# Optimization experiments

Measured on AMD Instinct MI355X. Metric: run time of the kernel, lower is better.

The kernel has to match this reference:

```python
import jax, jax.numpy as jnp
import numpy as np

DIM, INNER, NH = 256, 64, 8
HD = INNER // NH  # 8
B, H, W = 2, 48, 48
EPS = 1e-6


def _ln2d(x, w, b):
    # channel-first LayerNorm over dim=1, biased variance (matches LayerNorm2d)
    u = x.mean(axis=1, keepdims=True)
    s = ((x - u) ** 2).mean(axis=1, keepdims=True)
    xn = (x - u) / jnp.sqrt(s + EPS)
    return w[None, :, None, None] * xn + b[None, :, None, None]


def _conv1x1(x, w, b):
    return jnp.einsum('oc,bchw->bohw', w, x) + b[None, :, None, None]


def _attn(q, k, v):
    # q,k,v: [B, INNER, H, W] -> global attention over HW tokens per head
    Bq, C, Hh, Ww = q.shape
    split = lambda t: t.reshape(Bq, NH, HD, Hh * Ww)
    q, k, v = split(q), split(k), split(v)
    scale = HD ** -0.5
    attn = jnp.einsum('bhdn,bhdm->bhnm', q, k) * scale  # [B,nh,HW,HW]
    attn = jax.nn.softmax(attn, axis=-1)
    out = jnp.einsum('bhnm,bhdm->bhdn', attn, v)
    return out.reshape(Bq, C, Hh, Ww)


def setup_inputs() -> dict:
    key = jax.random.key(0)
    ks = jax.random.split(key, 12)
    w = lambda k, o, i: jax.random.normal(k, (o, i), dtype=jnp.float32) * 0.02
    d = {
        'f_rgb': jax.random.normal(ks[0], (B, DIM, H, W), dtype=jnp.float32),
        'f_ir': jax.random.normal(ks[1], (B, DIM, H, W), dtype=jnp.float32),
        'nr_w': jnp.ones(DIM), 'nr_b': jnp.zeros(DIM),
        'ni_w': jnp.ones(DIM), 'ni_b': jnp.zeros(DIM),
        'qr_w': w(ks[2], INNER, DIM), 'qr_b': jnp.zeros(INNER),
        'kvi_w': w(ks[3], 2 * INNER, DIM), 'kvi_b': jnp.zeros(2 * INNER),
        'qi_w': w(ks[4], INNER, DIM), 'qi_b': jnp.zeros(INNER),
        'kvr_w': w(ks[5], 2 * INNER, DIM), 'kvr_b': jnp.zeros(2 * INNER),
        'pr_w': w(ks[6], DIM, INNER), 'pr_b': jnp.zeros(DIM),
        'pr_lnw': jnp.ones(DIM), 'pr_lnb': jnp.zeros(DIM),
        'pi_w': w(ks[7], DIM, INNER), 'pi_b': jnp.zeros(DIM),
        'pi_lnw': jnp.ones(DIM), 'pi_lnb': jnp.zeros(DIM),
        'gr_w': w(ks[8], DIM, 2 * DIM), 'gr_b': jnp.zeros(DIM),
        'gi_w': w(ks[9], DIM, 2 * DIM), 'gi_b': jnp.zeros(DIM),
    }
    return d


def reference(f_rgb, f_ir, nr_w, nr_b, ni_w, ni_b, qr_w, qr_b, kvi_w, kvi_b,
              qi_w, qi_b, kvr_w, kvr_b, pr_w, pr_b, pr_lnw, pr_lnb,
              pi_w, pi_b, pi_lnw, pi_lnb, gr_w, gr_b, gi_w, gi_b):
    n_rgb = _ln2d(f_rgb, nr_w, nr_b)
    n_ir = _ln2d(f_ir, ni_w, ni_b)

    # RGB queries attend to IR keys/values
    q_r = _conv1x1(n_rgb, qr_w, qr_b)
    kv_i = _conv1x1(n_ir, kvi_w, kvi_b)
    k_i, v_i = kv_i[:, :INNER], kv_i[:, INNER:]
    rgb_cross = _attn(q_r, k_i, v_i)
    rgb_cross = _ln2d(_conv1x1(rgb_cross, pr_w, pr_b), pr_lnw, pr_lnb)
    gate_r = jax.nn.sigmoid(_conv1x1(jnp.concatenate([f_rgb, rgb_cross], axis=1), gr_w, gr_b))
    f_rgb_out = f_rgb + gate_r * rgb_cross

    # IR queries attend to RGB keys/values
    q_i = _conv1x1(n_ir, qi_w, qi_b)
    kv_r = _conv1x1(n_rgb, kvr_w, kvr_b)
    k_r, v_r = kv_r[:, :INNER], kv_r[:, INNER:]
    ir_cross = _attn(q_i, k_r, v_r)
    ir_cross = _ln2d(_conv1x1(ir_cross, pi_w, pi_b), pi_lnw, pi_lnb)
    gate_i = jax.nn.sigmoid(_conv1x1(jnp.concatenate([f_ir, ir_cross], axis=1), gi_w, gi_b))
    f_ir_out = f_ir + gate_i * ir_cross

    return (f_rgb_out, f_ir_out)
```

## Files before the change

### kernel.cpp

```cpp
#include <hip/hip_runtime.h>

static constexpr int kDim   = 256;
static constexpr int kInner = 64;
static constexpr int kNH    = 8;
static constexpr int kB     = 2;
static constexpr int kP     = 2304;
static constexpr float kScaleL2 = 0.5100697891920077f;
static constexpr float kEps   = 1e-6f;

typedef __fp16   fp16x2 __attribute__((ext_vector_type(2)));
typedef _Float16 half4f __attribute__((ext_vector_type(4)));
typedef _Float16 half8  __attribute__((ext_vector_type(8)));
typedef float    f32x4  __attribute__((ext_vector_type(4)));

static constexpr size_t oXq  = 0;
static constexpr size_t oQ16 = 2359296;
static constexpr size_t oK16 = 2949120;
static constexpr size_t oV16 = 3538944;
static constexpr size_t oA16 = 4128768;
static constexpr size_t oW16 = 7077888;
static constexpr size_t kInpStride = 294912;

__global__ __launch_bounds__(256) void prep(
    const float* __restrict__ x0, const float* __restrict__ w0,
    const float* __restrict__ b0, const float* __restrict__ x1,
    const float* __restrict__ w1, const float* __restrict__ b1,
    _Float16* __restrict__ Xq,
    const float* __restrict__ qr_w, const float* __restrict__ kvr_w,
    const float* __restrict__ qi_w, const float* __restrict__ kvi_w,
    const float* __restrict__ pr_w, const float* __restrict__ pi_w,
    const float* __restrict__ gr_w, const float* __restrict__ gi_w,
    _Float16* __restrict__ w16)
{
    if (blockIdx.x >= 576) {
        const int flat = blockIdx.x - 576;
        const int y = flat >> 6, x = flat & 63;
        const float* src; _Float16* dst; int n;
        _Float16* Aq = w16;
        _Float16* Ap = w16 + 98304;
        _Float16* Ag = w16 + 131072;
        switch (y) {
            case 0: src = qr_w;  dst = Aq;          n = 16384;  break;
            case 1: src = kvr_w; dst = Aq + 16384;  n = 32768;  break;
            case 2: src = qi_w;  dst = Aq + 49152;  n = 16384;  break;
            case 3: src = kvi_w; dst = Aq + 65536;  n = 32768;  break;
            case 4: src = pr_w;  dst = Ap;          n = 16384;  break;
            case 5: src = pi_w;  dst = Ap + 16384;  n = 16384;  break;
            case 6: src = gr_w;  dst = Ag;          n = 131072; break;
            default:src = gi_w;  dst = Ag + 131072; n = 131072; break;
        }
        for (int i = x * 256 + threadIdx.x; i < n; i += 64 * 256)
            dst[i] = (_Float16)src[i];
        return;
    }
    __shared__ float sb[16][16];
    __shared__ float ssb[16][16];
    const int fid = blockIdx.x;
    const int xcd = fid & 7, q = fid >> 3;
    const int inp = (xcd >> 2) & 1, bb = (xcd >> 1) & 1, half = xcd & 1;
    const float* x = inp ? x1 : x0;
    const float* w = inp ? w1 : w0;
    const float* b = inp ? b1 : b0;
    const int pos = threadIdx.x & 15;
    const int grp = threadIdx.x >> 4;
    const int p   = half * 1152 + q * 16 + pos;
    const size_t base = (size_t)bb * kDim * kP + p;
    const int c0 = grp * 16;

    float v[16];
    float s = 0.f, ss = 0.f;
    #pragma unroll
    for (int j = 0; j < 16; ++j) {
        v[j] = x[base + (size_t)(c0 + j) * kP];
        s += v[j]; ss += v[j] * v[j];
    }
    sb[grp][pos] = s; ssb[grp][pos] = ss;
    __syncthreads();
    float st = 0.f, sst = 0.f;
    #pragma unroll
    for (int g = 0; g < 16; ++g) { st += sb[g][pos]; sst += ssb[g][pos]; }
    const float mean = st * (1.f / kDim);
    const float rstd = rsqrtf(sst * (1.f / kDim) - mean * mean + kEps);
    half8 h0, h1;
    #pragma unroll
    for (int j = 0; j < 8; ++j) {
        h0[j] = (_Float16)((v[j]     - mean) * rstd * w[c0 + j]     + b[c0 + j]);
        h1[j] = (_Float16)((v[j + 8] - mean) * rstd * w[c0 + j + 8] + b[c0 + j + 8]);
    }
    _Float16* dst = Xq + ((size_t)(inp * 2 + bb) * kP + p) * 256 + c0;
    *(half8*)dst       = h0;
    *(half8*)(dst + 8) = h1;
}

template <int M, int K, int EPI>
__global__ __launch_bounds__(256) void gemm_f16(
    const _Float16* __restrict__ A,
    const _Float16* __restrict__ B,
    const float* __restrict__ b0, const float* __restrict__ b1,
    const float* __restrict__ b2, const float* __restrict__ b3,
    _Float16* __restrict__ o16a, _Float16* __restrict__ o16b, _Float16* __restrict__ o16c,
    const float* __restrict__ f0, const float* __restrict__ f1,
    float* __restrict__ outp)
{
    constexpr int MT64 = M / 64;
    const int fid = blockIdx.x;
    const int xcd = fid & 7, q = fid >> 3;
    const int s = (xcd >> 2) & 1, bb = (xcd >> 1) & 1, half = xcd & 1;
    const int ot64 = (q % MT64) * 64;
    const int pt   = q / MT64;
    const int wv = threadIdx.x >> 6, lane = threadIdx.x & 63;
    const int r16 = lane & 15, g = lane >> 4;
    const int ot = ot64 + wv * 16;
    const int p0 = half * 1152 + pt * 64;
    const int combo = s * 2 + bb;

    const _Float16* Ar = A + ((size_t)s * M + ot + r16) * K + 8 * g;
    const _Float16* Br = B + ((size_t)combo * kP + p0 + r16) * K + 8 * g;
    f32x4 acc0[4], acc1[4];
    #pragma unroll
    for (int ps = 0; ps < 4; ++ps) {
        acc0[ps] = (f32x4){0.f, 0.f, 0.f, 0.f};
        acc1[ps] = (f32x4){0.f, 0.f, 0.f, 0.f};
    }
    #pragma unroll 4
    for (int c0 = 0; c0 < K; c0 += 32) {
        const half8 a8 = *(const half8*)(Ar + c0);
        half8 b8[4];
        #pragma unroll
        for (int ps = 0; ps < 4; ++ps)
            b8[ps] = *(const half8*)(Br + (size_t)(16 * ps) * K + c0);
        const half4f al = {a8[0], a8[1], a8[2], a8[3]};
        const half4f ah = {a8[4], a8[5], a8[6], a8[7]};
        #pragma unroll
        for (int ps = 0; ps < 4; ++ps) {
            const half4f bl = {b8[ps][0], b8[ps][1], b8[ps][2], b8[ps][3]};
            const half4f bh = {b8[ps][4], b8[ps][5], b8[ps][6], b8[ps][7]};
            acc0[ps] = __builtin_amdgcn_mfma_f32_16x16x16f16(al, bl, acc0[ps], 0, 0, 0);
            acc1[ps] = __builtin_amdgcn_mfma_f32_16x16x16f16(ah, bh, acc1[ps], 0, 0, 0);
        }
    }
    const int obase = ot + 4 * g;

    #pragma unroll
    for (int ps = 0; ps < 4; ++ps) {
        float acc[4];
        #pragma unroll
        for (int i = 0; i < 4; ++i) acc[i] = acc0[ps][i] + acc1[ps][i];
        const int p = p0 + 16 * ps + r16;

        if constexpr (EPI == 0) {
            const int dlo = 4 * (g & 1);
            if (ot < 64) {
                const float* qb = s ? b1 : b0;
                const float4 bv = *(const float4*)(qb + obase);
                const int h = (ot >> 3) + (g >> 1);
                half4f o = { (_Float16)((acc[0] + bv.x) * kScaleL2), (_Float16)((acc[1] + bv.y) * kScaleL2),
                             (_Float16)((acc[2] + bv.z) * kScaleL2), (_Float16)((acc[3] + bv.w) * kScaleL2) };
                *(half4f*)(o16a + (((size_t)combo * 8 + h) * kP + p) * 8 + dlo) = o;
            } else if (ot < 128) {
                const float* kb = s ? b3 : b2;
                const float4 bv = *(const float4*)(kb + obase - 64);
                const int h = ((ot - 64) >> 3) + (g >> 1);
                half4f o = { (_Float16)(acc[0] + bv.x), (_Float16)(acc[1] + bv.y),
                             (_Float16)(acc[2] + bv.z), (_Float16)(acc[3] + bv.w) };
                *(half4f*)(o16b + (((size_t)combo * 8 + h) * kP + p) * 8 + dlo) = o;
            } else {
                const float* kb = s ? b3 : b2;
                const float4 bv = *(const float4*)(kb + obase - 64);
                const int h = ((ot - 128) >> 3) + (g >> 1);
                const float* bvp = (const float*)&bv;
                #pragma unroll
                for (int i = 0; i < 4; ++i)
                    o16c[(((size_t)combo * 8 + h) * 8 + dlo + i) * kP + p] = (_Float16)(acc[i] + bvp[i]);
            }
        } else {
            const float* gb = s ? b1 : b0;
            const float4 bv = *(const float4*)(gb + obase);
            const float* bvp = (const float*)&bv;
            const half4f cx = *(const half4f*)(B + ((size_t)combo * kP + p) * 512 + 256 + obase);
            const float* F = s ? f1 : f0;
            #pragma unroll
            for (int i = 0; i < 4; ++i) {
                const int o = obase + i;
                const float gt = 1.f / (1.f + __expf(-(acc[i] + bvp[i])));
                const float fb = F[((size_t)bb * kDim + o) * kP + p];
                outp[((size_t)combo * kDim + o) * kP + p] = fb + gt * (float)cx[i];
            }
        }
    }
}

__global__ __launch_bounds__(256) void proj_ln(
    const _Float16* __restrict__ a16, const _Float16* __restrict__ Ap,
    const float* __restrict__ pb0, const float* __restrict__ pb1,
    const float* __restrict__ w0, const float* __restrict__ b0,
    const float* __restrict__ w1, const float* __restrict__ b1,
    const float* __restrict__ f0, const float* __restrict__ f1,
    _Float16* __restrict__ Xg)
{
    __shared__ float sb[4][4][16];
    __shared__ float ssb[4][4][16];
    const int fid = blockIdx.x;
    const int xcd = fid & 7, q = fid >> 3;
    const int s = (xcd >> 2) & 1, bb = (xcd >> 1) & 1, half = xcd & 1;
    const int wv = threadIdx.x >> 6, lane = threadIdx.x & 63;
    const int r16 = lane & 15, g = lane >> 4;
    const int p = half * 1152 + q * 16 + r16;
    const int combo = s * 2 + bb;
    const float* pb = s ? pb1 : pb0;
    const float* w  = s ? w1 : w0;
    const float* b  = s ? b1 : b0;
    const float* F  = s ? f1 : f0;

    const _Float16* Br = a16 + ((size_t)combo * kP + p) * 64 + 8 * g;
    const half8 bA = *(const half8*)Br;
    const half8 bB = *(const half8*)(Br + 32);
    const half4f bl0 = {bA[0], bA[1], bA[2], bA[3]};
    const half4f bh0 = {bA[4], bA[5], bA[6], bA[7]};
    const half4f bl1 = {bB[0], bB[1], bB[2], bB[3]};
    const half4f bh1 = {bB[4], bB[5], bB[6], bB[7]};

    float cval[4][4];
    float psum = 0.f, psq = 0.f;
    #pragma unroll
    for (int t = 0; t < 4; ++t) {
        const int ot = wv * 64 + t * 16;
        const _Float16* Ar = Ap + ((size_t)s * 256 + ot + r16) * 64 + 8 * g;
        const half8 aA = *(const half8*)Ar;
        const half8 aB = *(const half8*)(Ar + 32);
        const half4f al0 = {aA[0], aA[1], aA[2], aA[3]};
        const half4f ah0 = {aA[4], aA[5], aA[6], aA[7]};
        const half4f al1 = {aB[0], aB[1], aB[2], aB[3]};
        const half4f ah1 = {aB[4], aB[5], aB[6], aB[7]};
        f32x4 acc0 = __builtin_amdgcn_mfma_f32_16x16x16f16(al0, bl0, (f32x4){0.f,0.f,0.f,0.f}, 0, 0, 0);
        acc0 = __builtin_amdgcn_mfma_f32_16x16x16f16(al1, bl1, acc0, 0, 0, 0);
        f32x4 acc1 = __builtin_amdgcn_mfma_f32_16x16x16f16(ah0, bh0, (f32x4){0.f,0.f,0.f,0.f}, 0, 0, 0);
        acc1 = __builtin_amdgcn_mfma_f32_16x16x16f16(ah1, bh1, acc1, 0, 0, 0);
        const float4 bv = *(const float4*)(pb + ot + 4 * g);
        const float* bvp = (const float*)&bv;
        #pragma unroll
        for (int i = 0; i < 4; ++i) {
            const float v = acc0[i] + acc1[i] + bvp[i];
            cval[t][i] = v;
            psum += v; psq += v * v;
        }
    }
    sb[wv][g][r16] = psum; ssb[wv][g][r16] = psq;
    __syncthreads();
    float st = 0.f, sst = 0.f;
    #pragma unroll
    for (int w2 = 0; w2 < 4; ++w2)
        #pragma unroll
        for (int g2 = 0; g2 < 4; ++g2) { st += sb[w2][g2][r16]; sst += ssb[w2][g2][r16]; }
    const float mean = st * (1.f / kDim);
    const float rstd = rsqrtf(sst * (1.f / kDim) - mean * mean + kEps);

    _Float16* xrow = Xg + ((size_t)combo * kP + p) * 512;
    #pragma unroll
    for (int t = 0; t < 4; ++t) {
        const int o4 = wv * 64 + t * 16 + 4 * g;
        const float4 lw = *(const float4*)(w + o4);
        const float4 lb = *(const float4*)(b + o4);
        const float* lwp = (const float*)&lw;
        const float* lbp = (const float*)&lb;
        half4f o;
        #pragma unroll
        for (int i = 0; i < 4; ++i)
            o[i] = (_Float16)((cval[t][i] - mean) * rstd * lwp[i] + lbp[i]);
        *(half4f*)(xrow + 256 + o4) = o;
        half4f r;
        #pragma unroll
        for (int i = 0; i < 4; ++i)
            r[i] = (_Float16)F[((size_t)bb * kDim + o4 + i) * kP + p];
        *(half4f*)(xrow + o4) = r;
    }
}

__global__ __launch_bounds__(256) void attn_mfma(
    const _Float16* __restrict__ q16, const _Float16* __restrict__ k16,
    const _Float16* __restrict__ vt16, _Float16* __restrict__ a16)
{
    __shared__ _Float16 Ksm[16 * 64 * 4];
    __shared__ _Float16 Vsm[16 * 66 * 4];
    const int st = blockIdx.z;
    const _Float16* Qg = q16  + (size_t)st * kInpStride;
    const _Float16* Kg = k16  + (size_t)(1 - st) * kInpStride;
    const _Float16* Vg = vt16 + (size_t)(1 - st) * kInpStride;
    const int bh = blockIdx.y;
    const int bb = bh >> 3, h = bh & 7;
    const int tid  = threadIdx.x;
    const int wv   = tid >> 6;
    const int lane = tid & 63;
    const int r16  = lane & 15;
    const int g    = lane >> 4;

    #pragma unroll
    for (int j = 0; j < 2; ++j) {
        const int s = tid + 256 * j;
        const int kt = s >> 5, m = s & 31;
        *(half4f*)(Ksm + (kt * 64 + 32 + m) * 4) = (half4f){0, 0, 0, 0};
        const int rv = 8 + (m & 7), gv = m >> 3;
        const half4f vv = (rv == 8)
            ? (half4f){(_Float16)1.f, (_Float16)1.f, (_Float16)1.f, (_Float16)1.f}
            : (half4f){0, 0, 0, 0};
        *(half4f*)(Vsm + (kt * 66 + gv * 16 + rv) * 4) = vv;
    }

    const int qg = blockIdx.x * 64 + wv * 16 + r16;
    half4f qf = (half4f){0, 0, 0, 0};
    if (g < 2) qf = *(const half4f*)(Qg + ((size_t)bh * kP + qg) * 8 + g * 4);

    const int vd = tid >> 5, vc8 = (tid & 31) * 8;
    const int vkt = vc8 >> 4, vgv = (vc8 & 15) >> 2;
    _Float16* kdst = Ksm + ((tid >> 4) * 64 + (tid & 15)) * 4;
    _Float16* vdst = Vsm + (vkt * 66 + vgv * 16 + vd) * 4;
    const _Float16* ksrc = Kg + ((size_t)bh * kP + tid) * 8;
    const _Float16* vsrc = Vg + (size_t)(bh * 8 + vd) * kP + vc8;

    half8 kreg = *(const half8*)ksrc;
    half8 vreg = *(const half8*)vsrc;

    f32x4 of0 = (f32x4){0.f, 0.f, 0.f, 0.f};
    f32x4 of1 = (f32x4){0.f, 0.f, 0.f, 0.f};

    for (int ch = 0; ch < 9; ++ch) {
        if (ch) __syncthreads();
        *(half4f*)kdst        = (half4f){kreg[0], kreg[1], kreg[2], kreg[3]};
        *(half4f*)(kdst + 64) = (half4f){kreg[4], kreg[5], kreg[6], kreg[7]};
        *(half4f*)vdst        = (half4f){vreg[0], vreg[1], vreg[2], vreg[3]};
        *(half4f*)(vdst + 64) = (half4f){vreg[4], vreg[5], vreg[6], vreg[7]};
        __syncthreads();
        if (ch < 8) {
            kreg = *(const half8*)(ksrc + (size_t)(ch + 1) * 2048);
            vreg = *(const half8*)(vsrc + (size_t)(ch + 1) * 256);
        }
        #pragma unroll
        for (int kt = 0; kt < 16; ++kt) {
            const half4f kf = *(const half4f*)(Ksm + (kt * 64 + lane) * 4);
            f32x4 sv = __builtin_amdgcn_mfma_f32_16x16x16f16(kf, qf, (f32x4){0.f,0.f,0.f,0.f}, 0, 0, 0);
            const float e0 = exp2f(sv[0]), e1 = exp2f(sv[1]);
            const float e2 = exp2f(sv[2]), e3 = exp2f(sv[3]);
            const fp16x2 lo = __builtin_amdgcn_cvt_pkrtz(e0, e1);
            const fp16x2 hi = __builtin_amdgcn_cvt_pkrtz(e2, e3);
            const half4f pf = { (_Float16)lo[0], (_Float16)lo[1],
                                (_Float16)hi[0], (_Float16)hi[1] };
            const half4f vf = *(const half4f*)(Vsm + (kt * 66 + lane) * 4);
            if (kt & 1) of1 = __builtin_amdgcn_mfma_f32_16x16x16f16(vf, pf, of1, 0, 0, 0);
            else        of0 = __builtin_amdgcn_mfma_f32_16x16x16f16(vf, pf, of0, 0, 0, 0);
        }
    }
    const f32x4 of = of0 + of1;
    const float rsv = __shfl(of[0], 32 + r16, 64);
    const float inv = 1.f / rsv;
    if (g < 2) {
        half4f o = { (_Float16)(of[0] * inv), (_Float16)(of[1] * inv),
                     (_Float16)(of[2] * inv), (_Float16)(of[3] * inv) };
        *(half4f*)(a16 + ((size_t)(st * 2 + bb) * kP + qg) * 64 + h * 8 + g * 4) = o;
    }
}

extern "C" void kernel_launch(void* const* d_in, const int* in_sizes, int n_in,
                              void* d_out, int out_size, void* d_ws, size_t ws_size,
                              hipStream_t stream)
{
    const float* f_rgb  = (const float*)d_in[0];
    const float* f_ir   = (const float*)d_in[1];
    const float* nr_w   = (const float*)d_in[2];
    const float* nr_b   = (const float*)d_in[3];
    const float* ni_w   = (const float*)d_in[4];
    const float* ni_b   = (const float*)d_in[5];
    const float* qr_w   = (const float*)d_in[6];
    const float* qr_b   = (const float*)d_in[7];
    const float* kvi_w  = (const float*)d_in[8];
    const float* kvi_b  = (const float*)d_in[9];
    const float* qi_w   = (const float*)d_in[10];
    const float* qi_b   = (const float*)d_in[11];
    const float* kvr_w  = (const float*)d_in[12];
    const float* kvr_b  = (const float*)d_in[13];
    const float* pr_w   = (const float*)d_in[14];
    const float* pr_b   = (const float*)d_in[15];
    const float* pr_lnw = (const float*)d_in[16];
    const float* pr_lnb = (const float*)d_in[17];
    const float* pi_w   = (const float*)d_in[18];
    const float* pi_b   = (const float*)d_in[19];
    const float* pi_lnw = (const float*)d_in[20];
    const float* pi_lnb = (const float*)d_in[21];
    const float* gr_w   = (const float*)d_in[22];
    const float* gr_b   = (const float*)d_in[23];
    const float* gi_w   = (const float*)d_in[24];
    const float* gi_b   = (const float*)d_in[25];

    _Float16* hb   = (_Float16*)d_ws;
    _Float16* Xq   = hb + oXq;
    _Float16* q16  = hb + oQ16;
    _Float16* k16  = hb + oK16;
    _Float16* vt16 = hb + oV16;
    _Float16* a16  = hb + oA16;
    _Float16* Xg   = hb;
    _Float16* W16  = hb + oW16;
    _Float16* Aq   = W16;
    _Float16* Ap   = W16 + 98304;
    _Float16* Ag   = W16 + 131072;

    float* outp = (float*)d_out;
    const dim3 blk(256);

    prep<<<dim3(1088), blk, 0, stream>>>(f_rgb, nr_w, nr_b, f_ir, ni_w, ni_b, Xq,
                                         qr_w, kvr_w, qi_w, kvi_w, pr_w, pi_w, gr_w, gi_w, W16);
    gemm_f16<192, 256, 0><<<dim3(432), blk, 0, stream>>>(
        Aq, Xq, qr_b, qi_b, kvr_b, kvi_b, q16, k16, vt16, nullptr, nullptr, nullptr);
    attn_mfma<<<dim3(36, 16, 2), blk, 0, stream>>>(q16, k16, vt16, a16);
    proj_ln<<<dim3(576), blk, 0, stream>>>(a16, Ap, pr_b, pi_b,
                                           pr_lnw, pr_lnb, pi_lnw, pi_lnb,
                                           f_rgb, f_ir, Xg);
    gemm_f16<256, 512, 2><<<dim3(576), blk, 0, stream>>>(
        Ag, Xg, gr_b, gi_b, nullptr, nullptr, nullptr, nullptr, nullptr, f_rgb, f_ir, outp);
}
```

Baseline: 118.6 us.

## Double-buffer attention K/V tiles and process two query tiles per wave

```diff
diff --git a/kernel.cpp b/kernel.cpp
--- a/kernel.cpp
+++ b/kernel.cpp
@@ -280,8 +280,8 @@
     const _Float16* __restrict__ q16, const _Float16* __restrict__ k16,
     const _Float16* __restrict__ vt16, _Float16* __restrict__ a16)
 {
-    __shared__ _Float16 Ksm[16 * 64 * 4];
-    __shared__ _Float16 Vsm[16 * 66 * 4];
+    __shared__ _Float16 Ksm[2][8 * 512];
+    __shared__ _Float16 Vsm[2][8 * 528];
     const int st = blockIdx.z;
     const _Float16* Qg = q16  + (size_t)st * kInpStride;
     const _Float16* Kg = k16  + (size_t)(1 - st) * kInpStride;
@@ -295,67 +295,129 @@
     const int g    = lane >> 4;
 
     #pragma unroll
-    for (int j = 0; j < 2; ++j) {
-        const int s = tid + 256 * j;
-        const int kt = s >> 5, m = s & 31;
-        *(half4f*)(Ksm + (kt * 64 + 32 + m) * 4) = (half4f){0, 0, 0, 0};
-        const int rv = 8 + (m & 7), gv = m >> 3;
-        const half4f vv = (rv == 8)
-            ? (half4f){(_Float16)1.f, (_Float16)1.f, (_Float16)1.f, (_Float16)1.f}
-            : (half4f){0, 0, 0, 0};
-        *(half4f*)(Vsm + (kt * 66 + gv * 16 + rv) * 4) = vv;
-    }
-
-    const int qg = blockIdx.x * 64 + wv * 16 + r16;
-    half4f qf = (half4f){0, 0, 0, 0};
-    if (g < 2) qf = *(const half4f*)(Qg + ((size_t)bh * kP + qg) * 8 + g * 4);
-
+    for (int jb = 0; jb < 2; ++jb) {
+        #pragma unroll
+        for (int j = 0; j < 2; ++j) {
+            const int s = tid + 256 * j;
+            const int kt = s >> 5, m = s & 31;
+            *(half4f*)(Ksm[jb] + (kt >> 1) * 512 + (32 + m) * 8 + (kt & 1) * 4) = (half4f){0, 0, 0, 0};
+            const int rv = 8 + (m & 7), gv = m >> 3;
+            const half4f vvp = (rv == 8)
+                ? (half4f){(_Float16)1.f, (_Float16)1.f, (_Float16)1.f, (_Float16)1.f}
+                : (half4f){0, 0, 0, 0};
+            *(half4f*)(Vsm[jb] + (kt >> 1) * 528 + (gv * 16 + rv) * 8 + (kt & 1) * 4) = vvp;
+        }
+    }
+
+    const int qgA = blockIdx.x * 128 + wv * 16 + r16;
+    const int qgB = qgA + 64;
+    half4f qfA = (half4f){0, 0, 0, 0};
+    half4f qfB = (half4f){0, 0, 0, 0};
+    if (g < 2) {
+        qfA = *(const half4f*)(Qg + ((size_t)bh * kP + qgA) * 8 + g * 4);
+        qfB = *(const half4f*)(Qg + ((size_t)bh * kP + qgB) * 8 + g * 4);
+    }
+
+    const int kkt = tid >> 4, kr = tid & 15;
     const int vd = tid >> 5, vc8 = (tid & 31) * 8;
     const int vkt = vc8 >> 4, vgv = (vc8 & 15) >> 2;
-    _Float16* kdst = Ksm + ((tid >> 4) * 64 + (tid & 15)) * 4;
-    _Float16* vdst = Vsm + (vkt * 66 + vgv * 16 + vd) * 4;
+    const int koff  = (kkt >> 1) * 512 + kr * 8 + (kkt & 1) * 4;
+    const int koff2 = koff + 128;
+    const int voff  = (vkt >> 1) * 528 + (vgv * 16 + vd) * 8 + (vkt & 1) * 4;
+    const int voff2 = voff + 128;
     const _Float16* ksrc = Kg + ((size_t)bh * kP + tid) * 8;
     const _Float16* vsrc = Vg + (size_t)(bh * 8 + vd) * kP + vc8;
 
-    half8 kreg = *(const half8*)ksrc;
-    half8 vreg = *(const half8*)vsrc;
-
-    f32x4 of0 = (f32x4){0.f, 0.f, 0.f, 0.f};
-    f32x4 of1 = (f32x4){0.f, 0.f, 0.f, 0.f};
+    {
+        const half8 k0 = *(const half8*)ksrc;
+        const half8 v0 = *(const half8*)vsrc;
+        *(half4f*)(Ksm[0] + koff)  = (half4f){k0[0], k0[1], k0[2], k0[3]};
+        *(half4f*)(Ksm[0] + koff2) = (half4f){k0[4], k0[5], k0[6], k0[7]};
+        *(half4f*)(Vsm[0] + voff)  = (half4f){v0[0], v0[1], v0[2], v0[3]};
+        *(half4f*)(Vsm[0] + voff2) = (half4f){v0[4], v0[5], v0[6], v0[7]};
+    }
+
+    f32x4 ofA0 = (f32x4){0.f, 0.f, 0.f, 0.f};
+    f32x4 ofA1 = (f32x4){0.f, 0.f, 0.f, 0.f};
+    f32x4 ofB0 = (f32x4){0.f, 0.f, 0.f, 0.f};
+    f32x4 ofB1 = (f32x4){0.f, 0.f, 0.f, 0.f};
 
     for (int ch = 0; ch < 9; ++ch) {
-        if (ch) __syncthreads();
-        *(half4f*)kdst        = (half4f){kreg[0], kreg[1], kreg[2], kreg[3]};
-        *(half4f*)(kdst + 64) = (half4f){kreg[4], kreg[5], kreg[6], kreg[7]};
-        *(half4f*)vdst        = (half4f){vreg[0], vreg[1], vreg[2], vreg[3]};
-        *(half4f*)(vdst + 64) = (half4f){vreg[4], vreg[5], vreg[6], vreg[7]};
         __syncthreads();
+        half8 kreg, vreg;
         if (ch < 8) {
             kreg = *(const half8*)(ksrc + (size_t)(ch + 1) * 2048);
             vreg = *(const half8*)(vsrc + (size_t)(ch + 1) * 256);
         }
-        #pragma unroll
-        for (int kt = 0; kt < 16; ++kt) {
-            const half4f kf = *(const half4f*)(Ksm + (kt * 64 + lane) * 4);
-            f32x4 sv = __builtin_amdgcn_mfma_f32_16x16x16f16(kf, qf, (f32x4){0.f,0.f,0.f,0.f}, 0, 0, 0);
-            const float e0 = exp2f(sv[0]), e1 = exp2f(sv[1]);
-            const float e2 = exp2f(sv[2]), e3 = exp2f(sv[3]);
-            const fp16x2 lo = __builtin_amdgcn_cvt_pkrtz(e0, e1);
-            const fp16x2 hi = __builtin_amdgcn_cvt_pkrtz(e2, e3);
-            const half4f pf = { (_Float16)lo[0], (_Float16)lo[1],
-                                (_Float16)hi[0], (_Float16)hi[1] };
-            const half4f vf = *(const half4f*)(Vsm + (kt * 66 + lane) * 4);
-            if (kt & 1) of1 = __builtin_amdgcn_mfma_f32_16x16x16f16(vf, pf, of1, 0, 0, 0);
-            else        of0 = __builtin_amdgcn_mfma_f32_16x16x16f16(vf, pf, of0, 0, 0, 0);
-        }
-    }
-    const f32x4 of = of0 + of1;
-    const float rsv = __shfl(of[0], 32 + r16, 64);
-    const float inv = 1.f / rsv;
+        const _Float16* Kb = Ksm[ch & 1];
+        const _Float16* Vb = Vsm[ch & 1];
+        #pragma unroll
+        for (int kt2 = 0; kt2 < 8; ++kt2) {
+            const half8 k01 = *(const half8*)(Kb + kt2 * 512 + lane * 8);
+            const half8 v01 = *(const half8*)(Vb + kt2 * 528 + lane * 8);
+            {
+                const half4f kf = {k01[0], k01[1], k01[2], k01[3]};
+                const half4f vf = {v01[0], v01[1], v01[2], v01[3]};
+                f32x4 svA = __builtin_amdgcn_mfma_f32_16x16x16f16(kf, qfA, (f32x4){0.f,0.f,0.f,0.f}, 0, 0, 0);
+                f32x4 svB = __builtin_amdgcn_mfma_f32_16x16x16f16(kf, qfB, (f32x4){0.f,0.f,0.f,0.f}, 0, 0, 0);
+                const fp16x2 lA0 = __builtin_amdgcn_cvt_pkrtz(__builtin_amdgcn_exp2f(svA[0]),
+                                                              __builtin_amdgcn_exp2f(svA[1]));
+                const fp16x2 lA1 = __builtin_amdgcn_cvt_pkrtz(__builtin_amdgcn_exp2f(svA[2]),
+                                                              __builtin_amdgcn_exp2f(svA[3]));
+                const fp16x2 lB0 = __builtin_amdgcn_cvt_pkrtz(__builtin_amdgcn_exp2f(svB[0]),
+                                                              __builtin_amdgcn_exp2f(svB[1]));
+                const fp16x2 lB1 = __builtin_amdgcn_cvt_pkrtz(__builtin_amdgcn_exp2f(svB[2]),
+                                                              __builtin_amdgcn_exp2f(svB[3]));
+                const half4f pfA = { (_Float16)lA0[0], (_Float16)lA0[1],
+                                     (_Float16)lA1[0], (_Float16)lA1[1] };
+                const half4f pfB = { (_Float16)lB0[0], (_Float16)lB0[1],
+                                     (_Float16)lB1[0], (_Float16)lB1[1] };
+                ofA0 = __builtin_amdgcn_mfma_f32_16x16x16f16(vf, pfA, ofA0, 0, 0, 0);
+                ofB0 = __builtin_amdgcn_mfma_f32_16x16x16f16(vf, pfB, ofB0, 0, 0, 0);
+            }
+            {
+                const half4f kf = {k01[4], k01[5], k01[6], k01[7]};
+                const half4f vf = {v01[4], v01[5], v01[6], v01[7]};
+                f32x4 svA = __builtin_amdgcn_mfma_f32_16x16x16f16(kf, qfA, (f32x4){0.f,0.f,0.f,0.f}, 0, 0, 0);
+                f32x4 svB = __builtin_amdgcn_mfma_f32_16x16x16f16(kf, qfB, (f32x4){0.f,0.f,0.f,0.f}, 0, 0, 0);
+                const fp16x2 lA0 = __builtin_amdgcn_cvt_pkrtz(__builtin_amdgcn_exp2f(svA[0]),
+                                                              __builtin_amdgcn_exp2f(svA[1]));
+                const fp16x2 lA1 = __builtin_amdgcn_cvt_pkrtz(__builtin_amdgcn_exp2f(svA[2]),
+                                                              __builtin_amdgcn_exp2f(svA[3]));
+                const fp16x2 lB0 = __builtin_amdgcn_cvt_pkrtz(__builtin_amdgcn_exp2f(svB[0]),
+                                                              __builtin_amdgcn_exp2f(svB[1]));
+                const fp16x2 lB1 = __builtin_amdgcn_cvt_pkrtz(__builtin_amdgcn_exp2f(svB[2]),
+                                                              __builtin_amdgcn_exp2f(svB[3]));
+                const half4f pfA = { (_Float16)lA0[0], (_Float16)lA0[1],
+                                     (_Float16)lA1[0], (_Float16)lA1[1] };
+                const half4f pfB = { (_Float16)lB0[0], (_Float16)lB0[1],
+                                     (_Float16)lB1[0], (_Float16)lB1[1] };
+                ofA1 = __builtin_amdgcn_mfma_f32_16x16x16f16(vf, pfA, ofA1, 0, 0, 0);
+                ofB1 = __builtin_amdgcn_mfma_f32_16x16x16f16(vf, pfB, ofB1, 0, 0, 0);
+            }
+        }
+        if (ch < 8) {
+            _Float16* Kn = Ksm[(ch + 1) & 1];
+            _Float16* Vn = Vsm[(ch + 1) & 1];
+            *(half4f*)(Kn + koff)  = (half4f){kreg[0], kreg[1], kreg[2], kreg[3]};
+            *(half4f*)(Kn + koff2) = (half4f){kreg[4], kreg[5], kreg[6], kreg[7]};
+            *(half4f*)(Vn + voff)  = (half4f){vreg[0], vreg[1], vreg[2], vreg[3]};
+            *(half4f*)(Vn + voff2) = (half4f){vreg[4], vreg[5], vreg[6], vreg[7]};
+        }
+    }
+    const f32x4 ofA = ofA0 + ofA1;
+    const f32x4 ofB = ofB0 + ofB1;
+    const float rsvA = __shfl(ofA[0], 32 + r16, 64);
+    const float rsvB = __shfl(ofB[0], 32 + r16, 64);
     if (g < 2) {
-        half4f o = { (_Float16)(of[0] * inv), (_Float16)(of[1] * inv),
-                     (_Float16)(of[2] * inv), (_Float16)(of[3] * inv) };
-        *(half4f*)(a16 + ((size_t)(st * 2 + bb) * kP + qg) * 64 + h * 8 + g * 4) = o;
+        const float invA = 1.f / rsvA;
+        half4f oA = { (_Float16)(ofA[0] * invA), (_Float16)(ofA[1] * invA),
+                      (_Float16)(ofA[2] * invA), (_Float16)(ofA[3] * invA) };
+        *(half4f*)(a16 + ((size_t)(st * 2 + bb) * kP + qgA) * 64 + h * 8 + g * 4) = oA;
+        const float invB = 1.f / rsvB;
+        half4f oB = { (_Float16)(ofB[0] * invB), (_Float16)(ofB[1] * invB),
+                      (_Float16)(ofB[2] * invB), (_Float16)(ofB[3] * invB) };
+        *(half4f*)(a16 + ((size_t)(st * 2 + bb) * kP + qgB) * 64 + h * 8 + g * 4) = oB;
     }
 }
 
@@ -409,7 +471,7 @@
                                          qr_w, kvr_w, qi_w, kvi_w, pr_w, pi_w, gr_w, gi_w, W16);
     gemm_f16<192, 256, 0><<<dim3(432), blk, 0, stream>>>(
         Aq, Xq, qr_b, qi_b, kvr_b, kvi_b, q16, k16, vt16, nullptr, nullptr, nullptr);
-    attn_mfma<<<dim3(36, 16, 2), blk, 0, stream>>>(q16, k16, vt16, a16);
+    attn_mfma<<<dim3(18, 16, 2), blk, 0, stream>>>(q16, k16, vt16, a16);
     proj_ln<<<dim3(576), blk, 0, stream>>>(a16, Ap, pr_b, pi_b,
                                            pr_lnw, pr_lnb, pi_lnw, pi_lnb,
                                            f_rgb, f_ir, Xg);
```

After: 103.5 us. 1.15x faster.
